# Kernel tuning notes

Hardware: AMD Instinct MI355X
Metric: run time of the kernel (lower is better)

The kernel has to match this reference:

```python
import jax, jax.numpy as jnp
import numpy as np

# Dims (match init_kwargs / input_specs)
N, N_REP, K, D = 8, 2048, 16, 3
C_IN, C_LIFT = 64, 64
C_MID = C_IN + C_LIFT   # 128
C_OUT = 128             # groups=C_OUT -> depthwise since C_MID == C_OUT
EPS = 1e-5


def setup_inputs() -> dict:
    key = jax.random.key(0)
    ks = jax.random.split(key, 10)
    w = lambda i, shape, fan_in: (jax.random.uniform(ks[i], shape, dtype=jnp.float32) * 2.0 - 1.0) / np.float32(np.sqrt(fan_in))
    return dict(
        p=jax.random.normal(ks[0], (N, N_REP, D), dtype=jnp.float32),
        P=jax.random.normal(ks[1], (N, N_REP, K, D), dtype=jnp.float32),
        F=jax.random.normal(ks[2], (N, N_REP, K, C_IN), dtype=jnp.float32),
        # BatchNorm over the D spatial channels (training-mode stats)
        bn_gamma=jnp.ones((D,), dtype=jnp.float32),
        bn_beta=jnp.zeros((D,), dtype=jnp.float32),
        # mlp_lift: Dense(D->C_LIFT) + Dense(C_LIFT->C_LIFT), ELU each
        lift_w1=w(3, (D, C_LIFT), D), lift_b1=jnp.zeros((C_LIFT,), dtype=jnp.float32),
        lift_w2=w(4, (C_LIFT, C_LIFT), C_LIFT), lift_b2=jnp.zeros((C_LIFT,), dtype=jnp.float32),
        # mid_conv: 1x1 Conv2d(D -> K) channels-last == Linear on last dim
        mid_w=w(5, (D, K), D), mid_b=jnp.zeros((K,), dtype=jnp.float32),
        # mlp: Dense(K->K) with ELU
        mlp_w=w(6, (K, K), K), mlp_b=jnp.zeros((K,), dtype=jnp.float32),
        # end_conv: Conv2d(C_MID -> C_OUT, kernel (K,1), groups=C_OUT) == depthwise
        # reduction over the neighbor dim; weight per (out_channel, neighbor)
        end_w=w(7, (C_OUT, K), K), end_b=jnp.zeros((C_OUT,), dtype=jnp.float32),
    )


def reference(p, P, F, bn_gamma, bn_beta, lift_w1, lift_b1, lift_w2, lift_b2,
              mid_w, mid_b, mlp_w, mlp_b, end_w, end_b):
    # Center neighborhoods on the representative point
    P_local = P - p[:, :, None, :]                              # (N,R,K,D)
    # Channels-last BatchNorm over D, batch stats over (N,R,K)
    mean = jnp.mean(P_local, axis=(0, 1, 2), keepdims=True)
    var = jnp.var(P_local, axis=(0, 1, 2), keepdims=True)
    P_norm = (P_local - mean) * jax.lax.rsqrt(var + EPS) * bn_gamma + bn_beta
    # Lift spatial coords to C_LIFT features (MLP of Dense+ELU layers)
    F_lift = jax.nn.elu(P_norm @ lift_w1 + lift_b1)
    F_lift = jax.nn.elu(F_lift @ lift_w2 + lift_b2)             # (N,R,K,C_LIFT)
    F_cat = jnp.concatenate([F_lift, F], axis=-1)               # (N,R,K,C_MID)
    # X-transform: 1x1 conv D->K then Dense(K->K)+ELU -> (N,R,K,K)
    X = P_norm @ mid_w + mid_b
    X = jax.nn.elu(X @ mlp_w + mlp_b)
    # Weighted aggregation: small batched matmul over the neighbor dim
    F_X = jnp.einsum('nrkj,nrjc->nrkc', X, F_cat)               # (N,R,K,C_MID)
    # Depthwise end conv: per-channel weighted sum over neighbors
    F_p = jnp.einsum('nrkc,ck->nrc', F_X, end_w) + end_b        # (N,R,C_OUT)
    return F_p
```

## Files before the change

kernel.cpp:

```cpp
#include <hip/hip_runtime.h>
#include <cstddef>

#define N_TOT   8
#define R_TOT   2048
#define NR_TOT  (N_TOT*R_TOT)
#define KK      16
#define CL      64
#define CM      128
#define EPSV    1e-5f
#define CNTF    262144.0f

typedef float  f32x4  __attribute__((ext_vector_type(4)));
typedef short  bf16x8 __attribute__((ext_vector_type(8)));

union FragU { bf16x8 f; unsigned u[4]; };

__device__ __forceinline__ float elu_f(float x){
    return x > 0.f ? x : (__expf(x) - 1.f);
}

#if defined(__has_builtin) && __has_builtin(__builtin_amdgcn_cvt_pk_bf16_f32)
__device__ __forceinline__ unsigned pk_bf16(float a, float b){
    auto v = __builtin_amdgcn_cvt_pk_bf16_f32(a, b);
    unsigned u; __builtin_memcpy(&u, &v, 4);
    return u;
}
#else
__device__ __forceinline__ unsigned pk_bf16(float a, float b){
    unsigned ua = __float_as_uint(a), ub = __float_as_uint(b);
    ua += 0x7fff + ((ua >> 16) & 1);
    ub += 0x7fff + ((ub >> 16) & 1);
    return (ua >> 16) | (ub & 0xffff0000u);
}
#endif
__device__ __forceinline__ float bf_lo(unsigned u){ return __uint_as_float(u << 16); }
__device__ __forceinline__ float bf_hi(unsigned u){ return __uint_as_float(u & 0xffff0000u); }

__device__ __forceinline__ void split4(const float* x, unsigned* o){
    unsigned h01 = pk_bf16(x[0], x[1]);
    unsigned h23 = pk_bf16(x[2], x[3]);
    float l0 = x[0] - bf_lo(h01), l1 = x[1] - bf_hi(h01);
    float l2 = x[2] - bf_lo(h23), l3 = x[3] - bf_hi(h23);
    o[0] = h01; o[1] = h23; o[2] = pk_bf16(l0, l1); o[3] = pk_bf16(l2, l3);
}

__global__ __launch_bounds__(256) void xconv_stats(
    const float* __restrict__ p, const float* __restrict__ P, float* __restrict__ ws)
{
    const int g = blockIdx.x*256 + threadIdx.x;
    const float4* P4 = (const float4*)(P + (size_t)g*12);
    float4 a = P4[0], b = P4[1], c = P4[2];
    const int nr = g >> 2;
    float pp0 = p[nr*3], pp1 = p[nr*3+1], pp2 = p[nr*3+2];
    float vx0=a.x-pp0, vx1=a.w-pp0, vx2=b.z-pp0, vx3=c.y-pp0;
    float vy0=a.y-pp1, vy1=b.x-pp1, vy2=b.w-pp1, vy3=c.z-pp1;
    float vz0=a.z-pp2, vz1=b.y-pp2, vz2=c.x-pp2, vz3=c.w-pp2;
    float s1[3], s2[3];
    s1[0]=vx0+vx1+vx2+vx3; s2[0]=vx0*vx0+vx1*vx1+vx2*vx2+vx3*vx3;
    s1[1]=vy0+vy1+vy2+vy3; s2[1]=vy0*vy0+vy1*vy1+vy2*vy2+vy3*vy3;
    s1[2]=vz0+vz1+vz2+vz3; s2[2]=vz0*vz0+vz1*vz1+vz2*vz2+vz3*vz3;

    #pragma unroll
    for (int off = 32; off > 0; off >>= 1){
        #pragma unroll
        for (int d = 0; d < 3; d++){
            s1[d] += __shfl_down(s1[d], off, 64);
            s2[d] += __shfl_down(s2[d], off, 64);
        }
    }
    __shared__ float red[4][6];
    int wave = threadIdx.x >> 6, lane = threadIdx.x & 63;
    if (lane == 0){
        #pragma unroll
        for (int d = 0; d < 3; d++){ red[wave][d] = s1[d]; red[wave][3+d] = s2[d]; }
    }
    __syncthreads();
    if (threadIdx.x < 6){
        float v = red[0][threadIdx.x] + red[1][threadIdx.x]
                + red[2][threadIdx.x] + red[3][threadIdx.x];
        atomicAdd(&ws[threadIdx.x], v);
    }
}

__global__ __launch_bounds__(256) void xconv_main(
    const float* __restrict__ p,   const float* __restrict__ P,
    const float* __restrict__ F,
    const float* __restrict__ gamma,const float* __restrict__ beta,
    const float* __restrict__ w1,  const float* __restrict__ b1,
    const float* __restrict__ w2,  const float* __restrict__ b2,
    const float* __restrict__ midw,const float* __restrict__ midb,
    const float* __restrict__ mlpw,const float* __restrict__ mlpb,
    const float* __restrict__ endw,const float* __restrict__ endb,
    const float* __restrict__ ws,  float* __restrict__ out)
{
    __shared__ float sEndw[128*20];

    const int tid  = threadIdx.x;
    const int lane = tid & 63;
    const int lo16 = lane & 15;
    const int quad = lane >> 4;
    const int wave = tid >> 6;

    {
        const float4* ep = (const float4*)endw;
        float4 v0 = ep[tid*2], v1 = ep[tid*2 + 1];
        int c = tid >> 1, k0 = (tid & 1) * 8;
        float* dst = &sEndw[c*20 + k0];
        *(float4*)dst = v0; *(float4*)(dst + 4) = v1;
    }
    __syncthreads();

    float sc[3], sh[3];
    #pragma unroll
    for (int d = 0; d < 3; d++){
        float mean = ws[d] / CNTF;
        float var  = ws[3+d] / CNTF - mean*mean;
        float s    = gamma[d] * rsqrtf(var + EPSV);
        sc[d] = s; sh[d] = beta[d] - mean*s;
    }

    unsigned w1pk[2][8][2];
    #pragma unroll
    for (int s = 0; s < 2; s++)
        #pragma unroll
        for (int j = 0; j < 8; j++){
            int q = s*32 + quad*8 + j;
            w1pk[s][j][0] = pk_bf16(w1[q],        w1[64 + q]);
            w1pk[s][j][1] = pk_bf16(w1[128 + q],  b1[q]);
        }
    FragU w2f[4][2];
    #pragma unroll
    for (int b = 0; b < 4; b++)
        #pragma unroll
        for (int s = 0; s < 2; s++)
            #pragma unroll
            for (int d = 0; d < 4; d++){
                int q0 = s*32 + quad*8 + d*2;
                int idx = q0*64 + b*16 + lo16;
                w2f[b][s].u[d] = pk_bf16(w2[idx], w2[idx + 64]);
            }
    FragU mlpA[2];
    {
        float mw[4];
        #pragma unroll
        for (int r = 0; r < 4; r++) mw[r] = mlpw[(quad*4 + r)*16 + lo16];
        unsigned o[4]; split4(mw, o);
        mlpA[0].u[0]=o[0]; mlpA[0].u[1]=o[1]; mlpA[0].u[2]=o[0]; mlpA[0].u[3]=o[1];
        mlpA[1].u[0]=o[2]; mlpA[1].u[1]=o[3]; mlpA[1].u[2]=o[2]; mlpA[1].u[3]=o[3];
    }
    float mlpbr[4];
    #pragma unroll
    for (int r = 0; r < 4; r++) mlpbr[r] = mlpb[quad*4 + r];
    float mw0[4], mw1[4], mw2[4], mbv[4];
    #pragma unroll
    for (int j = 0; j < 4; j++){
        int m2 = quad*4 + j;
        mw0[j] = midw[m2]; mw1[j] = midw[16 + m2]; mw2[j] = midw[32 + m2];
        mbv[j] = midb[m2];
    }
    float b2r[4];
    #pragma unroll
    for (int b = 0; b < 4; b++) b2r[b] = b2[b*16 + lo16];
    const float endb0 = endb[lane], endb1 = endb[64 + lane];

    const int wglobal = blockIdx.x*4 + wave;

    float nP0, nP1, nP2, npp0, npp1, npp2;
    {
        const int nr0 = wglobal*4;
        const int pb  = nr0*48 + lo16*3;
        nP0 = P[pb]; nP1 = P[pb+1]; nP2 = P[pb+2];
        npp0 = p[nr0*3]; npp1 = p[nr0*3+1]; npp2 = p[nr0*3+2];
    }

    #pragma unroll 1
    for (int it = 0; it < 4; it++){
        const int nr = wglobal*4 + it;

        const float P0 = nP0, P1 = nP1, P2 = nP2;
        const float pp0 = npp0, pp1 = npp1, pp2 = npp2;

        float fv[4][4];
        #pragma unroll
        for (int bt = 0; bt < 4; bt++)
            #pragma unroll
            for (int r = 0; r < 4; r++)
                fv[bt][r] = F[(size_t)nr*1024 + (quad*4 + r)*64 + bt*16 + lo16];

        if (it < 3){
            const int nn = nr + 1;
            const int pb = nn*48 + lo16*3;
            nP0 = P[pb]; nP1 = P[pb+1]; nP2 = P[pb+2];
            npp0 = p[nn*3]; npp1 = p[nn*3+1]; npp2 = p[nn*3+2];
        }

        const float pn0 = (P0 - pp0)*sc[0] + sh[0];
        const float pn1 = (P1 - pp1)*sc[1] + sh[1];
        const float pn2 = (P2 - pp2)*sc[2] + sh[2];

        FragU hf[2];
        #pragma unroll
        for (int s = 0; s < 2; s++)
            #pragma unroll
            for (int d = 0; d < 4; d++){
                float e[2];
                #pragma unroll
                for (int h2 = 0; h2 < 2; h2++){
                    unsigned pa = w1pk[s][2*d + h2][0], pbk = w1pk[s][2*d + h2][1];
                    float h = bf_hi(pbk);
                    h = fmaf(pn0, bf_lo(pa), h);
                    h = fmaf(pn1, bf_hi(pa), h);
                    h = fmaf(pn2, bf_lo(pbk), h);
                    e[h2] = elu_f(h);
                }
                hf[s].u[d] = pk_bf16(e[0], e[1]);
            }

        float x0[4];
        #pragma unroll
        for (int j = 0; j < 4; j++)
            x0[j] = fmaf(pn2, mw2[j], fmaf(pn1, mw1[j], fmaf(pn0, mw0[j], mbv[j])));
        FragU x0f; split4(x0, x0f.u);

        f32x4 dx = {0.f,0.f,0.f,0.f};
        dx = __builtin_amdgcn_mfma_f32_16x16x32_bf16(mlpA[0].f, x0f.f, dx, 0,0,0);
        dx = __builtin_amdgcn_mfma_f32_16x16x32_bf16(mlpA[1].f, x0f.f, dx, 0,0,0);
        float xv[4];
        #pragma unroll
        for (int r = 0; r < 4; r++) xv[r] = elu_f(dx[r] + mlpbr[r]);
        FragU xA; split4(xv, xA.u);

        float o0 = 0.f, o1 = 0.f;

        #pragma unroll
        for (int b = 0; b < 4; b++){
            f32x4 dl = {0.f,0.f,0.f,0.f};
            dl = __builtin_amdgcn_mfma_f32_16x16x32_bf16(hf[0].f, w2f[b][0].f, dl, 0,0,0);
            dl = __builtin_amdgcn_mfma_f32_16x16x32_bf16(hf[1].f, w2f[b][1].f, dl, 0,0,0);
            float fl[4];
            #pragma unroll
            for (int r = 0; r < 4; r++) fl[r] = elu_f(dl[r] + b2r[b]);
            FragU bfg;
            unsigned h01 = pk_bf16(fl[0], fl[1]), h23 = pk_bf16(fl[2], fl[3]);
            bfg.u[0] = h01; bfg.u[1] = h23; bfg.u[2] = h01; bfg.u[3] = h23;
            f32x4 da = {0.f,0.f,0.f,0.f};
            da = __builtin_amdgcn_mfma_f32_16x16x32_bf16(xA.f, bfg.f, da, 0,0,0);
            const float4 ew = *(const float4*)&sEndw[(b*16 + lo16)*20 + quad*4];
            float pt = da[0]*ew.x + da[1]*ew.y + da[2]*ew.z + da[3]*ew.w;
            pt += __shfl_xor(pt, 16, 64);
            pt += __shfl_xor(pt, 32, 64);
            if (b == quad) o0 = pt;
        }
        #pragma unroll
        for (int bt = 0; bt < 4; bt++){
            FragU bfg;
            unsigned h01 = pk_bf16(fv[bt][0], fv[bt][1]);
            unsigned h23 = pk_bf16(fv[bt][2], fv[bt][3]);
            bfg.u[0] = h01; bfg.u[1] = h23; bfg.u[2] = h01; bfg.u[3] = h23;
            f32x4 da = {0.f,0.f,0.f,0.f};
            da = __builtin_amdgcn_mfma_f32_16x16x32_bf16(xA.f, bfg.f, da, 0,0,0);
            const float4 ew = *(const float4*)&sEndw[(64 + bt*16 + lo16)*20 + quad*4];
            float pt = da[0]*ew.x + da[1]*ew.y + da[2]*ew.z + da[3]*ew.w;
            pt += __shfl_xor(pt, 16, 64);
            pt += __shfl_xor(pt, 32, 64);
            if (bt == quad) o1 = pt;
        }

        out[(size_t)nr*CM + lane]      = o0 + endb0;
        out[(size_t)nr*CM + 64 + lane] = o1 + endb1;
    }
}

extern "C" void kernel_launch(void* const* d_in, const int* in_sizes, int n_in,
                              void* d_out, int out_size, void* d_ws, size_t ws_size,
                              hipStream_t stream)
{
    const float* p     = (const float*)d_in[0];
    const float* P     = (const float*)d_in[1];
    const float* F     = (const float*)d_in[2];
    const float* gamma = (const float*)d_in[3];
    const float* beta  = (const float*)d_in[4];
    const float* w1    = (const float*)d_in[5];
    const float* b1    = (const float*)d_in[6];
    const float* w2    = (const float*)d_in[7];
    const float* b2    = (const float*)d_in[8];
    const float* midw  = (const float*)d_in[9];
    const float* midb  = (const float*)d_in[10];
    const float* mlpw  = (const float*)d_in[11];
    const float* mlpb  = (const float*)d_in[12];
    const float* endw  = (const float*)d_in[13];
    const float* endb  = (const float*)d_in[14];
    float* ws  = (float*)d_ws;
    float* out = (float*)d_out;

    hipMemsetAsync(d_ws, 0, 32, stream);
    xconv_stats<<<256, 256, 0, stream>>>(p, P, ws);
    xconv_main <<<1024, 256, 0, stream>>>(p, P, F, gamma, beta, w1, b1, w2, b2,
                                          midw, midb, mlpw, mlpb, endw, endb, ws, out);
}
```

Before: 147.7 us.

## Stage weights in LDS and software-pipeline front/back halves across iterations

Moves the packed bf16 lift weights (w1, w2) out of per-thread registers into shared memory, filled cooperatively by different waves, and reads them from LDS inside the loop. It also splits each iteration into a front stage (loads, lift layer 1, X-transform) and a back stage (lift layer 2, aggregation, output), running the front of the next item before the back of the current one to overlap global loads with MFMA work. This lowers register pressure from the preloaded weight fragments and hides load latency. In exchange it adds LDS traffic per iteration and keeps two pipeline states live at once.

```diff
diff --git a/kernel.cpp b/kernel.cpp
--- a/kernel.cpp
+++ b/kernel.cpp
@@ -10,8 +10,10 @@
 #define EPSV    1e-5f
 #define CNTF    262144.0f
 
-typedef float  f32x4  __attribute__((ext_vector_type(4)));
-typedef short  bf16x8 __attribute__((ext_vector_type(8)));
+typedef float    f32x4  __attribute__((ext_vector_type(4)));
+typedef short    bf16x8 __attribute__((ext_vector_type(8)));
+typedef unsigned u32x2  __attribute__((ext_vector_type(2)));
+typedef unsigned u32x4  __attribute__((ext_vector_type(4)));
 
 union FragU { bf16x8 f; unsigned u[4]; };
 
@@ -82,6 +84,8 @@
     }
 }
 
+struct PS { FragU hf[2]; FragU xA; float fv[4][4]; int nr; };
+
 __global__ __launch_bounds__(256) void xconv_main(
     const float* __restrict__ p,   const float* __restrict__ P,
     const float* __restrict__ F,
@@ -93,7 +97,9 @@
     const float* __restrict__ endw,const float* __restrict__ endb,
     const float* __restrict__ ws,  float* __restrict__ out)
 {
-    __shared__ float sEndw[128*20];
+    __shared__ float    sEndw[128*20];
+    __shared__ unsigned sW1[2*64*20];
+    __shared__ unsigned sW2[8*64*4];
 
     const int tid  = threadIdx.x;
     const int lane = tid & 63;
@@ -101,14 +107,38 @@
     const int quad = lane >> 4;
     const int wave = tid >> 6;
 
-    {
+    if (wave == 0){
+        #pragma unroll
+        for (int s = 0; s < 2; s++)
+            #pragma unroll
+            for (int j = 0; j < 8; j++){
+                int q = s*32 + quad*8 + j;
+                u32x2 v;
+                v.x = pk_bf16(w1[q],       w1[64 + q]);
+                v.y = pk_bf16(w1[128 + q], b1[q]);
+                *(u32x2*)&sW1[(s*64 + lane)*20 + j*2] = v;
+            }
+    } else if (wave == 1){
+        #pragma unroll
+        for (int b = 0; b < 4; b++)
+            #pragma unroll
+            for (int s = 0; s < 2; s++){
+                u32x4 f;
+                #pragma unroll
+                for (int d = 0; d < 4; d++){
+                    int q0 = s*32 + quad*8 + d*2;
+                    int idx = q0*64 + b*16 + lo16;
+                    f[d] = pk_bf16(w2[idx], w2[idx + 64]);
+                }
+                *(u32x4*)&sW2[((b*2 + s)*64 + lane)*4] = f;
+            }
+    } else {
+        int c = tid - 128;
         const float4* ep = (const float4*)endw;
-        float4 v0 = ep[tid*2], v1 = ep[tid*2 + 1];
-        int c = tid >> 1, k0 = (tid & 1) * 8;
-        float* dst = &sEndw[c*20 + k0];
-        *(float4*)dst = v0; *(float4*)(dst + 4) = v1;
-    }
-    __syncthreads();
+        #pragma unroll
+        for (int i = 0; i < 4; i++)
+            *(float4*)&sEndw[c*20 + i*4] = ep[c*4 + i];
+    }
 
     float sc[3], sh[3];
     #pragma unroll
@@ -118,27 +148,6 @@
         float s    = gamma[d] * rsqrtf(var + EPSV);
         sc[d] = s; sh[d] = beta[d] - mean*s;
     }
-
-    unsigned w1pk[2][8][2];
-    #pragma unroll
-    for (int s = 0; s < 2; s++)
-        #pragma unroll
-        for (int j = 0; j < 8; j++){
-            int q = s*32 + quad*8 + j;
-            w1pk[s][j][0] = pk_bf16(w1[q],        w1[64 + q]);
-            w1pk[s][j][1] = pk_bf16(w1[128 + q],  b1[q]);
-        }
-    FragU w2f[4][2];
-    #pragma unroll
-    for (int b = 0; b < 4; b++)
-        #pragma unroll
-        for (int s = 0; s < 2; s++)
-            #pragma unroll
-            for (int d = 0; d < 4; d++){
-                int q0 = s*32 + quad*8 + d*2;
-                int idx = q0*64 + b*16 + lo16;
-                w2f[b][s].u[d] = pk_bf16(w2[idx], w2[idx + 64]);
-            }
     FragU mlpA[2];
     {
         float mw[4];
@@ -163,80 +172,64 @@
     for (int b = 0; b < 4; b++) b2r[b] = b2[b*16 + lo16];
     const float endb0 = endb[lane], endb1 = endb[64 + lane];
 
-    const int wglobal = blockIdx.x*4 + wave;
-
-    float nP0, nP1, nP2, npp0, npp1, npp2;
-    {
-        const int nr0 = wglobal*4;
-        const int pb  = nr0*48 + lo16*3;
-        nP0 = P[pb]; nP1 = P[pb+1]; nP2 = P[pb+2];
-        npp0 = p[nr0*3]; npp1 = p[nr0*3+1]; npp2 = p[nr0*3+2];
-    }
-
-    #pragma unroll 1
-    for (int it = 0; it < 4; it++){
-        const int nr = wglobal*4 + it;
-
-        const float P0 = nP0, P1 = nP1, P2 = nP2;
-        const float pp0 = npp0, pp1 = npp1, pp2 = npp2;
-
-        float fv[4][4];
+    __syncthreads();
+
+    auto front = [&](int nr, PS& S){
+        S.nr = nr;
         #pragma unroll
         for (int bt = 0; bt < 4; bt++)
             #pragma unroll
             for (int r = 0; r < 4; r++)
-                fv[bt][r] = F[(size_t)nr*1024 + (quad*4 + r)*64 + bt*16 + lo16];
-
-        if (it < 3){
-            const int nn = nr + 1;
-            const int pb = nn*48 + lo16*3;
-            nP0 = P[pb]; nP1 = P[pb+1]; nP2 = P[pb+2];
-            npp0 = p[nn*3]; npp1 = p[nn*3+1]; npp2 = p[nn*3+2];
-        }
-
+                S.fv[bt][r] = F[(size_t)nr*1024 + (quad*4 + r)*64 + bt*16 + lo16];
+
+        const int pb = nr*48 + lo16*3;
+        float P0 = P[pb], P1 = P[pb+1], P2 = P[pb+2];
+        float pp0 = p[nr*3], pp1 = p[nr*3+1], pp2 = p[nr*3+2];
         const float pn0 = (P0 - pp0)*sc[0] + sh[0];
         const float pn1 = (P1 - pp1)*sc[1] + sh[1];
         const float pn2 = (P2 - pp2)*sc[2] + sh[2];
 
-        FragU hf[2];
-        #pragma unroll
-        for (int s = 0; s < 2; s++)
+        #pragma unroll
+        for (int s = 0; s < 2; s++){
+            const u32x4* wp = (const u32x4*)&sW1[(s*64 + lane)*20];
             #pragma unroll
             for (int d = 0; d < 4; d++){
-                float e[2];
-                #pragma unroll
-                for (int h2 = 0; h2 < 2; h2++){
-                    unsigned pa = w1pk[s][2*d + h2][0], pbk = w1pk[s][2*d + h2][1];
-                    float h = bf_hi(pbk);
-                    h = fmaf(pn0, bf_lo(pa), h);
-                    h = fmaf(pn1, bf_hi(pa), h);
-                    h = fmaf(pn2, bf_lo(pbk), h);
-                    e[h2] = elu_f(h);
-                }
-                hf[s].u[d] = pk_bf16(e[0], e[1]);
+                u32x4 w = wp[d];
+                float h0 = bf_hi(w.y);
+                h0 = fmaf(pn0, bf_lo(w.x), h0);
+                h0 = fmaf(pn1, bf_hi(w.x), h0);
+                h0 = fmaf(pn2, bf_lo(w.y), h0);
+                float h1v = bf_hi(w.w);
+                h1v = fmaf(pn0, bf_lo(w.z), h1v);
+                h1v = fmaf(pn1, bf_hi(w.z), h1v);
+                h1v = fmaf(pn2, bf_lo(w.w), h1v);
+                S.hf[s].u[d] = pk_bf16(elu_f(h0), elu_f(h1v));
             }
-
+        }
         float x0[4];
         #pragma unroll
         for (int j = 0; j < 4; j++)
             x0[j] = fmaf(pn2, mw2[j], fmaf(pn1, mw1[j], fmaf(pn0, mw0[j], mbv[j])));
         FragU x0f; split4(x0, x0f.u);
-
         f32x4 dx = {0.f,0.f,0.f,0.f};
         dx = __builtin_amdgcn_mfma_f32_16x16x32_bf16(mlpA[0].f, x0f.f, dx, 0,0,0);
         dx = __builtin_amdgcn_mfma_f32_16x16x32_bf16(mlpA[1].f, x0f.f, dx, 0,0,0);
         float xv[4];
         #pragma unroll
         for (int r = 0; r < 4; r++) xv[r] = elu_f(dx[r] + mlpbr[r]);
-        FragU xA; split4(xv, xA.u);
-
+        split4(xv, S.xA.u);
+    };
+
+    auto back = [&](PS& S){
         float o0 = 0.f, o1 = 0.f;
-
         #pragma unroll
         for (int b = 0; b < 4; b++){
+            FragU wf0, wf1;
+            *(u32x4*)wf0.u = *(const u32x4*)&sW2[((b*2 + 0)*64 + lane)*4];
+            *(u32x4*)wf1.u = *(const u32x4*)&sW2[((b*2 + 1)*64 + lane)*4];
             f32x4 dl = {0.f,0.f,0.f,0.f};
-            dl = __builtin_amdgcn_mfma_f32_16x16x32_bf16(hf[0].f, w2f[b][0].f, dl, 0,0,0);
-            dl = __builtin_amdgcn_mfma_f32_16x16x32_bf16(hf[1].f, w2f[b][1].f, dl, 0,0,0);
+            dl = __builtin_amdgcn_mfma_f32_16x16x32_bf16(S.hf[0].f, wf0.f, dl, 0,0,0);
+            dl = __builtin_amdgcn_mfma_f32_16x16x32_bf16(S.hf[1].f, wf1.f, dl, 0,0,0);
             float fl[4];
             #pragma unroll
             for (int r = 0; r < 4; r++) fl[r] = elu_f(dl[r] + b2r[b]);
@@ -244,7 +237,7 @@
             unsigned h01 = pk_bf16(fl[0], fl[1]), h23 = pk_bf16(fl[2], fl[3]);
             bfg.u[0] = h01; bfg.u[1] = h23; bfg.u[2] = h01; bfg.u[3] = h23;
             f32x4 da = {0.f,0.f,0.f,0.f};
-            da = __builtin_amdgcn_mfma_f32_16x16x32_bf16(xA.f, bfg.f, da, 0,0,0);
+            da = __builtin_amdgcn_mfma_f32_16x16x32_bf16(S.xA.f, bfg.f, da, 0,0,0);
             const float4 ew = *(const float4*)&sEndw[(b*16 + lo16)*20 + quad*4];
             float pt = da[0]*ew.x + da[1]*ew.y + da[2]*ew.z + da[3]*ew.w;
             pt += __shfl_xor(pt, 16, 64);
@@ -254,21 +247,32 @@
         #pragma unroll
         for (int bt = 0; bt < 4; bt++){
             FragU bfg;
-            unsigned h01 = pk_bf16(fv[bt][0], fv[bt][1]);
-            unsigned h23 = pk_bf16(fv[bt][2], fv[bt][3]);
+            unsigned h01 = pk_bf16(S.fv[bt][0], S.fv[bt][1]);
+            unsigned h23 = pk_bf16(S.fv[bt][2], S.fv[bt][3]);
             bfg.u[0] = h01; bfg.u[1] = h23; bfg.u[2] = h01; bfg.u[3] = h23;
             f32x4 da = {0.f,0.f,0.f,0.f};
-            da = __builtin_amdgcn_mfma_f32_16x16x32_bf16(xA.f, bfg.f, da, 0,0,0);
+            da = __builtin_amdgcn_mfma_f32_16x16x32_bf16(S.xA.f, bfg.f, da, 0,0,0);
             const float4 ew = *(const float4*)&sEndw[(64 + bt*16 + lo16)*20 + quad*4];
             float pt = da[0]*ew.x + da[1]*ew.y + da[2]*ew.z + da[3]*ew.w;
             pt += __shfl_xor(pt, 16, 64);
             pt += __shfl_xor(pt, 32, 64);
             if (bt == quad) o1 = pt;
         }
-
-        out[(size_t)nr*CM + lane]      = o0 + endb0;
-        out[(size_t)nr*CM + 64 + lane] = o1 + endb1;
-    }
+        out[(size_t)S.nr*CM + lane]      = o0 + endb0;
+        out[(size_t)S.nr*CM + 64 + lane] = o1 + endb1;
+    };
+
+    const int base = (blockIdx.x*4 + wave) * 4;
+
+    PS S; front(base, S);
+    #pragma unroll 1
+    for (int it = 0; it < 3; it++){
+        PS T;
+        front(base + it + 1, T);
+        back(S);
+        S = T;
+    }
+    back(S);
 }
 
 extern "C" void kernel_launch(void* const* d_in, const int* in_sizes, int n_in,
```

New measurement: 151.2 us. 2.4% more time.
